# Optimization experiments

Measured on AMD Instinct MI355X. Metric: run time of the kernel, lower is better.

## Reference

```python
import jax, jax.numpy as jnp
import numpy as np

B, T, C, H, NT = 1, 1024, 768, 12, 8
D = C // H  # 64
POWER_ITERS = 4
DP_TEMP = 0.8
ESR_GAMMA = 0.02
ESR_ALPHA = 0.1


def rmsnorm(x, w, eps=1e-6):
    rms = jax.lax.rsqrt(jnp.mean(x * x, axis=-1, keepdims=True) + eps)
    return x * rms * w


def setup_inputs():
    key = jax.random.key(0)
    k0, k1, k2 = jax.random.split(key, 3)
    return {
        "x": jax.random.normal(k0, (B, T, C), jnp.float32),
        "W_qkvg": jax.random.normal(k1, (4 * C, C), jnp.float32) * 0.02,
        "W_out": jax.random.normal(k2, (C, C), jnp.float32) * 0.02,
        "lam": jnp.float32(1.5),
        "log_tau": -0.5 * jnp.ones((H, NT), jnp.float32),
        "logit_w": jnp.zeros((H, NT), jnp.float32),
        "beta": 1.5 * jnp.ones((H,), jnp.float32),
        "out_scale": jnp.ones((H,), jnp.float32),
        "dp_scale": jnp.ones((H,), jnp.float32),
        "logk_scale": jnp.ones((H,), jnp.float32),
        "dt_logit": jnp.float32(np.log(1.0 / 1e-8)),  # dt=1.0 -> logit = log(dt/(1-dt+1e-8))
        "g_norm_w": jnp.ones((D,), jnp.float32),
    }


def reference(x, W_qkvg, W_out, lam, log_tau, logit_w, beta, out_scale,
              dp_scale, logk_scale, dt_logit, g_norm_w):
    # qkvg projection and head split
    qkvg = x @ W_qkvg.T                                    # [B,T,4C]
    q, k, v, g = jnp.split(qkvg, 4, axis=-1)
    to_heads = lambda t: t.reshape(B, T, H, D).transpose(0, 2, 1, 3)  # [B,H,T,D]
    q, k, v, g = map(to_heads, (q, k, v, g))
    g = rmsnorm(g, g_norm_w)

    # pairwise squared distance ||g_i - g_j||^2
    g2 = jnp.sum(g * g, axis=-1)                           # [B,H,T]
    s = jnp.maximum(g2[..., :, None] + g2[..., None, :]
                    - 2.0 * jnp.einsum('bhid,bhjd->bhij', g, g), 0.0)  # [B,H,T,T]

    # fractional log-kernel: logsumexp_t[-(beta/2) log1p(s/(4 tau_t)) + log w_t]
    tau = jnp.maximum(jnp.exp(log_tau), 1e-6)              # [H,NT]
    w = jax.nn.softmax(logit_w, axis=-1)                   # [H,NT]
    beta_c = jnp.clip(beta, 0.5, 2.5)                      # [H]
    log_k_per = -(beta_c[None, :, None, None, None] / 2.0) * jnp.log1p(
        s[:, :, None] / (4.0 * tau[None, :, :, None, None]))          # [B,H,NT,T,T]
    logK = jax.nn.logsumexp(log_k_per + jnp.log(w + 1e-12)[None, :, :, None, None], axis=2)
    logK = logK * logk_scale[None, :, None, None]

    # dot-product scores
    dp = jnp.einsum('bhid,bhjd->bhij', q, k) * (dp_scale[None, :, None, None]
                                                / (np.sqrt(D) * DP_TEMP))

    # causal Markov normalize: blend, mask, stable row-softmax
    mask = jnp.tril(jnp.ones((T, T), bool))[None, None]    # [1,1,T,T]
    blended = lam * dp + (1.0 - lam) * logK
    blended = jnp.where(mask, blended, -jnp.inf)
    mx = jnp.max(blended, axis=-1, keepdims=True)
    mx = jnp.where(jnp.isfinite(mx), mx, 0.0)
    Kmat = jnp.exp(jnp.maximum(blended - mx, -60.0)) * mask
    P = Kmat / jnp.maximum(Kmat.sum(-1, keepdims=True), 1e-12)

    # power iteration for left stationary pi with full-support teleport
    pi0 = jnp.full((B, H, 1, T), 1.0 / T, P.dtype)
    def step(pi, _):
        p = (1.0 - ESR_GAMMA) * (pi @ P) + ESR_GAMMA / T
        p = p / jnp.maximum(p.sum(-1, keepdims=True), 1e-12)
        return p, None
    pi, _ = jax.lax.scan(step, pi0, None, length=POWER_ITERS)
    pi = jax.lax.stop_gradient(pi[..., 0, :])              # [B,H,T] (detached)

    # causal approximation to additive reversibilization
    P_adj = (pi[..., None, :] / jnp.maximum(pi[..., :, None], 1e-12)) \
            * jnp.swapaxes(P, -1, -2)                      # P*_ij = (pi_j/pi_i) P_ji
    P_rev = 0.5 * (P + P_adj) * mask
    P_rev = P_rev / jnp.maximum(P_rev.sum(-1, keepdims=True), 1e-12)

    dt = jax.nn.sigmoid(dt_logit)
    alpha = ESR_ALPHA * dt                                  # scale_alpha_by_dt=True
    P_fin = (1.0 - alpha) * P + alpha * P_rev

    y = (P_fin @ v) * out_scale[None, :, None, None]       # [B,H,T,D]
    y = y.transpose(0, 2, 1, 3).reshape(B, T, C)
    return y @ W_out.T
```

## Files before the change

kernel.cpp:

```cpp
#include <hip/hip_runtime.h>
#include <math.h>

#define TSEQ 1024
#define CD   768
#define HN   12
#define DD   64

#define OFF_QH     0
#define OFF_KH     393216
#define OFF_GH     786432
#define OFF_VHT    1179648
#define OFF_VH     1572864
#define OFF_G2     1966080
#define OFF_YB     1978368
#define OFF_CONSTS 2371584
#define OFF_OPART  2372096
#define OFF_LS     8663552
#define OFF_PD     8761856
#define OFF_XB     8774144
#define OFF_WQB    9167360
#define OFF_WOB    10347008

#define N_XB  786432
#define N_WQB 2359296
#define N_WOB 589824

typedef __bf16 bf16x8 __attribute__((ext_vector_type(8)));
typedef float  f32x4  __attribute__((ext_vector_type(4)));
typedef unsigned short u16x8 __attribute__((ext_vector_type(8)));
typedef unsigned short u16x4 __attribute__((ext_vector_type(4)));

__device__ inline unsigned short f2bf(float f) {
  unsigned int u = __float_as_uint(f);
  return (unsigned short)((u + 0x7fffu + ((u >> 16) & 1u)) >> 16);
}
__device__ inline float bf2f(unsigned short u) {
  return __uint_as_float((unsigned)u << 16);
}


__global__ __launch_bounds__(64) void prep_kernel(
    const float* __restrict__ lam_p, const float* __restrict__ log_tau,
    const float* __restrict__ logit_w, const float* __restrict__ beta,
    const float* __restrict__ out_scale, const float* __restrict__ dp_scale,
    const float* __restrict__ logk_scale, const float* __restrict__ dt_logit,
    float* __restrict__ consts) {
  int h = threadIdx.x;
  if (h == 0) {
    float dt = 1.0f / (1.0f + __expf(-dt_logit[0]));
    consts[288] = 0.1f * dt;
  }
  if (h < HN) {
    float lam = lam_p[0];
    float* c = consts + h * 24;
    c[0] = lam * dp_scale[h] * (1.0f / 6.4f);
    c[1] = (1.0f - lam) * logk_scale[h];
    float b = fminf(fmaxf(beta[h], 0.5f), 2.5f);
    c[2] = 0.5f * b;
    c[3] = out_scale[h];
    float m = -1e30f;
    float lw[8];
    bool uni = true;
    for (int t = 0; t < 8; t++) {
      lw[t] = logit_w[h * 8 + t];
      m = fmaxf(m, lw[t]);
      if (log_tau[h * 8 + t] != log_tau[h * 8] || lw[t] != lw[0]) uni = false;
    }
    float s = 0.f;
    float e[8];
    for (int t = 0; t < 8; t++) { e[t] = __expf(lw[t] - m); s += e[t]; }
    for (int t = 0; t < 8; t++) {
      float w = e[t] / s;
      c[12 + t] = log2f(w + 1e-12f);
      float tau = fmaxf(__expf(log_tau[h * 8 + t]), 1e-6f);
      c[4 + t] = 1.0f / (4.0f * tau);
    }
    c[20] = uni ? 1.0f : 8.0f;
  }
}

__global__ __launch_bounds__(256) void convert_kernel(
    const float* __restrict__ x, const float* __restrict__ wq,
    const float* __restrict__ wo, unsigned short* __restrict__ xb,
    unsigned short* __restrict__ wqb, unsigned short* __restrict__ wob) {
  int i8 = (blockIdx.x * 256 + threadIdx.x) * 8;
  const float* src;
  unsigned short* dst;
  int off;
  if (i8 < N_XB) { src = x; dst = xb; off = i8; }
  else if (i8 < N_XB + N_WQB) { src = wq; dst = wqb; off = i8 - N_XB; }
  else if (i8 < N_XB + N_WQB + N_WOB) { src = wo; dst = wob; off = i8 - N_XB - N_WQB; }
  else return;
  float4 a = *(const float4*)&src[off];
  float4 b = *(const float4*)&src[off + 4];
  u16x8 u;
  u[0] = f2bf(a.x); u[1] = f2bf(a.y); u[2] = f2bf(a.z); u[3] = f2bf(a.w);
  u[4] = f2bf(b.x); u[5] = f2bf(b.y); u[6] = f2bf(b.z); u[7] = f2bf(b.w);
  *(u16x8*)&dst[off] = u;
}

__global__ __launch_bounds__(256, 2) void gemm_qkvg_fused(
    const unsigned short* __restrict__ A, const unsigned short* __restrict__ B,
    const float* __restrict__ consts, const float* __restrict__ g_norm_w,
    unsigned short* __restrict__ qh, unsigned short* __restrict__ kh,
    unsigned short* __restrict__ gh, unsigned short* __restrict__ vh,
    unsigned short* __restrict__ vhT, float* __restrict__ g2) {
  const int K = 768;
  __shared__ __align__(16) unsigned short As[128 * 72];
  __shared__ __align__(16) unsigned short Bs[64 * 72];
  int t = threadIdx.x;
  int lane = t & 63, w = t >> 6;
  int quad = lane >> 4, tx = lane & 15;
  int n0 = blockIdx.x * 64, m0 = blockIdx.y * 128;

  f32x4 acc[2][4] = {};
  int r_ = t >> 3, c8 = (t & 7) * 8;

  for (int k0 = 0; k0 < K; k0 += 64) {
    __syncthreads();
#pragma unroll
    for (int rep = 0; rep < 4; rep++) {
      int r = rep * 32 + r_;
      *(u16x8*)&As[r * 72 + c8] = *(const u16x8*)&A[(size_t)(m0 + r) * K + k0 + c8];
    }
#pragma unroll
    for (int rep = 0; rep < 2; rep++) {
      int r = rep * 32 + r_;
      *(u16x8*)&Bs[r * 72 + c8] = *(const u16x8*)&B[(size_t)(n0 + r) * K + k0 + c8];
    }
    __syncthreads();

#pragma unroll
    for (int ks = 0; ks < 2; ks++) {
      bf16x8 af[2];
#pragma unroll
      for (int mi = 0; mi < 2; mi++)
        af[mi] = *(const bf16x8*)&As[(32 * w + mi * 16 + tx) * 72 + ks * 32 + quad * 8];
#pragma unroll
      for (int ni = 0; ni < 4; ni++) {
        bf16x8 bv = *(const bf16x8*)&Bs[(ni * 16 + tx) * 72 + ks * 32 + quad * 8];
#pragma unroll
        for (int mi = 0; mi < 2; mi++)
          acc[mi][ni] = __builtin_amdgcn_mfma_f32_16x16x32_bf16(af[mi], bv, acc[mi][ni], 0, 0, 0);
      }
    }
  }

  int typ = n0 / CD;
  int h = (n0 - typ * CD) >> 6;
  unsigned short* Ls = As;
  __syncthreads();

  if (typ == 3) {
    float gw4[4];
#pragma unroll
    for (int ni = 0; ni < 4; ni++) gw4[ni] = g_norm_w[ni * 16 + tx];
#pragma unroll
    for (int mi = 0; mi < 2; mi++) {
#pragma unroll
      for (int reg = 0; reg < 4; reg++) {
        float s1 = acc[mi][0][reg] * acc[mi][0][reg] + acc[mi][1][reg] * acc[mi][1][reg]
                 + acc[mi][2][reg] * acc[mi][2][reg] + acc[mi][3][reg] * acc[mi][3][reg];
#pragma unroll
        for (int m = 1; m < 16; m <<= 1) s1 += __shfl_xor(s1, m, 64);
        float rms = rsqrtf(s1 * (1.f / 64.f) + 1e-6f);
        int rl = 32 * w + mi * 16 + quad * 4 + reg;
        float s2 = 0.f;
#pragma unroll
        for (int ni = 0; ni < 4; ni++) {
          float v = acc[mi][ni][reg] * rms * gw4[ni];
          unsigned short us = f2bf(v);
          Ls[rl * 72 + ni * 16 + tx] = us;
          float vb = bf2f(us);
          s2 += vb * vb;
        }
#pragma unroll
        for (int m = 1; m < 16; m <<= 1) s2 += __shfl_xor(s2, m, 64);
        if (tx == 0) g2[h * 1024 + m0 + rl] = s2;
      }
    }
    __syncthreads();
#pragma unroll
    for (int rep = 0; rep < 4; rep++) {
      int idx = rep * 256 + t;
      int r = idx >> 3, cc = (idx & 7) * 8;
      *(u16x8*)&gh[(size_t)(h * 1024 + m0 + r) * 64 + cc] = *(const u16x8*)&Ls[r * 72 + cc];
    }
  } else {
    float sc = (typ == 0) ? consts[h * 24] * 1.44269504089f : 1.0f;
#pragma unroll
    for (int mi = 0; mi < 2; mi++)
#pragma unroll
      for (int ni = 0; ni < 4; ni++)
#pragma unroll
        for (int reg = 0; reg < 4; reg++) {
          int rl = 32 * w + mi * 16 + quad * 4 + reg;
          Ls[rl * 72 + ni * 16 + tx] = f2bf(acc[mi][ni][reg] * sc);
        }
    __syncthreads();
    unsigned short* dst = (typ == 0) ? qh : ((typ == 1) ? kh : vh);
#pragma unroll
    for (int rep = 0; rep < 4; rep++) {
      int idx = rep * 256 + t;
      int r = idx >> 3, cc = (idx & 7) * 8;
      *(u16x8*)&dst[(size_t)(h * 1024 + m0 + r) * 64 + cc] = *(const u16x8*)&Ls[r * 72 + cc];
    }
    if (typ == 2) {
#pragma unroll
      for (int rep = 0; rep < 4; rep++) {
        int idx = rep * 256 + t;
        int d = idx >> 4, rc = (idx & 15) * 8;
        u16x8 u;
#pragma unroll
        for (int j = 0; j < 8; j++) u[j] = Ls[(rc + j) * 72 + d];
        *(u16x8*)&vhT[(size_t)(h * 64 + d) * 1024 + m0 + rc] = u;
      }
    }
  }
}

__global__ __launch_bounds__(256, 2) void gemm_bf16_abT(
    const unsigned short* __restrict__ A, const unsigned short* __restrict__ B,
    float* __restrict__ Cm, int M, int N, int K) {
  __shared__ __align__(16) unsigned short As[128 * 72];
  __shared__ __align__(16) unsigned short Bs[64 * 72];
  int t = threadIdx.x;
  int lane = t & 63, w = t >> 6;
  int quad = lane >> 4, tx = lane & 15;
  int n0 = blockIdx.x * 64, m0 = blockIdx.y * 128;

  f32x4 acc[2][4] = {};
  int r_ = t >> 3, c8 = (t & 7) * 8;

  for (int k0 = 0; k0 < K; k0 += 64) {
    __syncthreads();
#pragma unroll
    for (int rep = 0; rep < 4; rep++) {
      int r = rep * 32 + r_;
      *(u16x8*)&As[r * 72 + c8] = *(const u16x8*)&A[(size_t)(m0 + r) * K + k0 + c8];
    }
#pragma unroll
    for (int rep = 0; rep < 2; rep++) {
      int r = rep * 32 + r_;
      *(u16x8*)&Bs[r * 72 + c8] = *(const u16x8*)&B[(size_t)(n0 + r) * K + k0 + c8];
    }
    __syncthreads();

#pragma unroll
    for (int ks = 0; ks < 2; ks++) {
      bf16x8 af[2];
#pragma unroll
      for (int mi = 0; mi < 2; mi++)
        af[mi] = *(const bf16x8*)&As[(32 * w + mi * 16 + tx) * 72 + ks * 32 + quad * 8];
#pragma unroll
      for (int ni = 0; ni < 4; ni++) {
        bf16x8 bv = *(const bf16x8*)&Bs[(ni * 16 + tx) * 72 + ks * 32 + quad * 8];
#pragma unroll
        for (int mi = 0; mi < 2; mi++)
          acc[mi][ni] = __builtin_amdgcn_mfma_f32_16x16x32_bf16(af[mi], bv, acc[mi][ni], 0, 0, 0);
      }
    }
  }

#pragma unroll
  for (int mi = 0; mi < 2; mi++)
#pragma unroll
    for (int ni = 0; ni < 4; ni++)
#pragma unroll
      for (int reg = 0; reg < 4; reg++) {
        int row = m0 + 32 * w + mi * 16 + quad * 4 + reg;
        Cm[(size_t)row * N + n0 + ni * 16 + tx] = acc[mi][ni][reg];
      }
}

__global__ __launch_bounds__(256, 3) void flash_kernel(
    const unsigned short* __restrict__ qh, const unsigned short* __restrict__ kh,
    const unsigned short* __restrict__ gh, const unsigned short* __restrict__ vhT,
    const float* __restrict__ g2, const float* __restrict__ consts,
    float* __restrict__ Opart, float* __restrict__ lsp, float* __restrict__ pdp) {
  int h = blockIdx.y;
  int uu = 143 - (int)blockIdx.x;
  int it = 0, rem = uu;
  for (it = 0; it < 32; ++it) {
    int njt_ = (it >> 1) + 1;
    int nc = (njt_ + 1) >> 1;
    if (rem < nc) break;
    rem -= nc;
  }
  int njt = (it >> 1) + 1;
  int jt0 = rem * 2;
  int jt1 = (jt0 + 2 < njt) ? (jt0 + 2) : njt;
  bool owns_diag = (jt1 == njt);
  int i0 = it * 32;
  int t = threadIdx.x;
  int lane = t & 63, w = t >> 6;
  int quad = lane >> 4, tx = lane & 15;
  int mi = w >> 1, nb = (w & 1) * 2;

  __shared__ __align__(16) unsigned short Qa[32 * 72];
  __shared__ __align__(16) unsigned short Ga[32 * 72];
  __shared__ __align__(16) unsigned short Ks[64 * 72];
  __shared__ __align__(16) unsigned short Gjs[64 * 72];
  __shared__ __align__(16) unsigned short Vt[64 * 72];
  __shared__ __align__(16) unsigned short psh[32 * 72];
  __shared__ float g2i[32], g2j[64], pdiag[32], lsum[32];

  const float* ch = consts + h * 24;
  float lkc = ch[1], bh2 = ch[2];
  int ntt = (int)ch[20];
  float i4t0 = ch[4];
  float inv4tau[8], logw[8];
#pragma unroll
  for (int tt = 0; tt < 8; tt++) { inv4tau[tt] = ch[4 + tt]; logw[tt] = ch[12 + tt]; }

  {
    int r = t >> 3, c8 = (t & 7) * 8;
    *(u16x8*)&Qa[r * 72 + c8] = *(const u16x8*)&qh[(size_t)(h * 1024 + i0 + r) * 64 + c8];
    *(u16x8*)&Ga[r * 72 + c8] = *(const u16x8*)&gh[(size_t)(h * 1024 + i0 + r) * 64 + c8];
  }
  if (t < 32) { g2i[t] = g2[h * 1024 + i0 + t]; pdiag[t] = 0.f; }
  __syncthreads();

  bf16x8 aq[2], ag[2];
#pragma unroll
  for (int ks = 0; ks < 2; ks++) {
    aq[ks] = *(const bf16x8*)&Qa[(mi * 16 + tx) * 72 + ks * 32 + quad * 8];
    ag[ks] = *(const bf16x8*)&Ga[(mi * 16 + tx) * 72 + ks * 32 + quad * 8];
  }

  f32x4 Oc[2] = {};
  float rowacc[4] = {0.f, 0.f, 0.f, 0.f};
  int r4 = t >> 2, cb = (t & 3) * 16;

  for (int jt = jt0; jt < jt1; jt++) {
    int j0 = jt * 64;
    __syncthreads();
    {
      const unsigned short* kp = &kh[(size_t)(h * 1024 + j0 + r4) * 64 + cb];
      const unsigned short* gp = &gh[(size_t)(h * 1024 + j0 + r4) * 64 + cb];
      const unsigned short* vp = &vhT[(size_t)(h * 64 + r4) * 1024 + j0 + cb];
      *(u16x8*)&Ks[r4 * 72 + cb] = *(const u16x8*)kp;
      *(u16x8*)&Ks[r4 * 72 + cb + 8] = *(const u16x8*)(kp + 8);
      *(u16x8*)&Gjs[r4 * 72 + cb] = *(const u16x8*)gp;
      *(u16x8*)&Gjs[r4 * 72 + cb + 8] = *(const u16x8*)(gp + 8);
      *(u16x8*)&Vt[r4 * 72 + cb] = *(const u16x8*)vp;
      *(u16x8*)&Vt[r4 * 72 + cb + 8] = *(const u16x8*)(vp + 8);
    }
    if (t < 64) g2j[t] = g2[h * 1024 + j0 + t];
    __syncthreads();

    f32x4 sqk[2] = {}, sgg[2] = {};
#pragma unroll
    for (int ni2 = 0; ni2 < 2; ni2++) {
#pragma unroll
      for (int ks = 0; ks < 2; ks++) {
        bf16x8 bk = *(const bf16x8*)&Ks[((nb + ni2) * 16 + tx) * 72 + ks * 32 + quad * 8];
        sqk[ni2] = __builtin_amdgcn_mfma_f32_16x16x32_bf16(aq[ks], bk, sqk[ni2], 0, 0, 0);
        bf16x8 bg = *(const bf16x8*)&Gjs[((nb + ni2) * 16 + tx) * 72 + ks * 32 + quad * 8];
        sgg[ni2] = __builtin_amdgcn_mfma_f32_16x16x32_bf16(ag[ks], bg, sgg[ni2], 0, 0, 0);
      }
    }

    float rs[4] = {0.f, 0.f, 0.f, 0.f};
#pragma unroll
    for (int ni2 = 0; ni2 < 2; ni2++) {
      int colg = j0 + (nb + ni2) * 16 + tx;
      float g2jv = g2j[(nb + ni2) * 16 + tx];
#pragma unroll
      for (int reg = 0; reg < 4; reg++) {
        int rowl = mi * 16 + quad * 4 + reg;
        int gi = i0 + rowl;
        float s = fmaxf(g2i[rowl] + g2jv - 2.0f * sgg[ni2][reg], 0.0f);
        float lse2;
        if (ntt == 1) {
          lse2 = -bh2 * __builtin_amdgcn_logf(fmaf(s, i4t0, 1.0f));
        } else {
          float se = 0.f;
#pragma unroll
          for (int tt = 0; tt < 8; tt++) {
            float lv = __builtin_amdgcn_logf(fmaf(s, inv4tau[tt], 1.0f));
            se += __builtin_amdgcn_exp2f(fmaf(-bh2, lv, logw[tt]));
          }
          lse2 = __builtin_amdgcn_logf(se + 1e-30f);
        }
        float b = fmaf(lkc, lse2, sqk[ni2][reg]);
        float p = (colg <= gi) ? __builtin_amdgcn_exp2f(b) : 0.0f;
        rs[reg] += p;
        psh[rowl * 72 + (nb + ni2) * 16 + tx] = f2bf(p);
        if (colg == gi) pdiag[rowl] = p;
      }
    }
#pragma unroll
    for (int reg = 0; reg < 4; reg++) {
#pragma unroll
      for (int m = 1; m < 16; m <<= 1) rs[reg] += __shfl_xor(rs[reg], m, 64);
      rowacc[reg] += rs[reg];
    }
    __syncthreads();

    bf16x8 ap[2];
#pragma unroll
    for (int ks = 0; ks < 2; ks++)
      ap[ks] = *(const bf16x8*)&psh[(mi * 16 + tx) * 72 + ks * 32 + quad * 8];
#pragma unroll
    for (int nd2 = 0; nd2 < 2; nd2++) {
#pragma unroll
      for (int ks = 0; ks < 2; ks++) {
        bf16x8 bv = *(const bf16x8*)&Vt[((nb + nd2) * 16 + tx) * 72 + ks * 32 + quad * 8];
        Oc[nd2] = __builtin_amdgcn_mfma_f32_16x16x32_bf16(ap[ks], bv, Oc[nd2], 0, 0, 0);
      }
    }
  }

  if ((w & 1) == 0 && tx == 0) {
#pragma unroll
    for (int reg = 0; reg < 4; reg++) lsum[mi * 16 + quad * 4 + reg] = rowacc[reg];
  }
  __syncthreads();
  if ((w & 1) == 1 && tx == 0) {
#pragma unroll
    for (int reg = 0; reg < 4; reg++) {
      int rowl = mi * 16 + quad * 4 + reg;
      lsp[(size_t)(rem * HN + h) * 1024 + i0 + rowl] = lsum[rowl] + rowacc[reg];
    }
  }
  float* Ob = Opart + (size_t)((rem * HN + h) * 1024 + i0) * 64;
#pragma unroll
  for (int nd2 = 0; nd2 < 2; nd2++) {
#pragma unroll
    for (int reg = 0; reg < 4; reg++) {
      int rowl = mi * 16 + quad * 4 + reg;
      Ob[rowl * 64 + (nb + nd2) * 16 + tx] = Oc[nd2][reg];
    }
  }
  if (owns_diag && t < 32) pdp[h * 1024 + i0 + t] = pdiag[t];
}

__global__ __launch_bounds__(256) void finalize_kernel(
    const float* __restrict__ Opart, const float* __restrict__ lsp,
    const float* __restrict__ pdp, const unsigned short* __restrict__ vh,
    const float* __restrict__ consts, unsigned short* __restrict__ yb) {
  int h = blockIdx.y;
  int t = threadIdx.x;
  int rl = t >> 4, d4 = t & 15;
  int gi = blockIdx.x * 16 + rl;
  int it = gi >> 5;
  int nc = (((it >> 1) + 1) + 1) >> 1;
  float alpha = consts[288];
  float osc = consts[h * 24 + 3];
  float4 Ov = make_float4(0.f, 0.f, 0.f, 0.f);
  float l = 0.f;
  for (int c = 0; c < nc; c++) {
    float4 p = *(const float4*)&Opart[(size_t)((c * HN + h) * 1024 + gi) * 64 + 4 * d4];
    Ov.x += p.x; Ov.y += p.y; Ov.z += p.z; Ov.w += p.w;
    l += lsp[(size_t)(c * HN + h) * 1024 + gi];
  }
  l = fmaxf(l, 1e-12f);
  float Pii = pdp[h * TSEQ + gi] / l;
  float inv1p = 1.0f / (1.0f + Pii);
  float c1 = (1.0f - alpha) + alpha * inv1p;
  float c2 = alpha * Pii * inv1p;
  float invl = 1.0f / l;
  u16x4 vb = *(const u16x4*)&vh[(size_t)(h * 1024 + gi) * 64 + 4 * d4];
  u16x4 o;
  o[0] = f2bf(osc * (c1 * Ov.x * invl + c2 * bf2f(vb[0])));
  o[1] = f2bf(osc * (c1 * Ov.y * invl + c2 * bf2f(vb[1])));
  o[2] = f2bf(osc * (c1 * Ov.z * invl + c2 * bf2f(vb[2])));
  o[3] = f2bf(osc * (c1 * Ov.w * invl + c2 * bf2f(vb[3])));
  *(u16x4*)&yb[(size_t)gi * CD + h * 64 + 4 * d4] = o;
}

extern "C" void kernel_launch(void* const* d_in, const int* in_sizes, int n_in,
                              void* d_out, int out_size, void* d_ws, size_t ws_size,
                              hipStream_t stream) {
  (void)in_sizes; (void)n_in; (void)out_size; (void)ws_size;
  const float* x          = (const float*)d_in[0];
  const float* W_qkvg     = (const float*)d_in[1];
  const float* W_out      = (const float*)d_in[2];
  const float* lam        = (const float*)d_in[3];
  const float* log_tau    = (const float*)d_in[4];
  const float* logit_w    = (const float*)d_in[5];
  const float* beta       = (const float*)d_in[6];
  const float* out_scale  = (const float*)d_in[7];
  const float* dp_scale   = (const float*)d_in[8];
  const float* logk_scale = (const float*)d_in[9];
  const float* dt_logit   = (const float*)d_in[10];
  const float* g_norm_w   = (const float*)d_in[11];
  float* ws = (float*)d_ws;
  unsigned short* qh  = (unsigned short*)(ws + OFF_QH);
  unsigned short* kh  = (unsigned short*)(ws + OFF_KH);
  unsigned short* gh  = (unsigned short*)(ws + OFF_GH);
  unsigned short* vhT = (unsigned short*)(ws + OFF_VHT);
  unsigned short* vh  = (unsigned short*)(ws + OFF_VH);
  float* g2     = ws + OFF_G2;
  unsigned short* yb  = (unsigned short*)(ws + OFF_YB);
  float* consts = ws + OFF_CONSTS;
  float* Opart  = ws + OFF_OPART;
  float* lsp    = ws + OFF_LS;
  float* pdp    = ws + OFF_PD;
  unsigned short* xb  = (unsigned short*)(ws + OFF_XB);
  unsigned short* wqb = (unsigned short*)(ws + OFF_WQB);
  unsigned short* wob = (unsigned short*)(ws + OFF_WOB);
  float* out = (float*)d_out;

  prep_kernel<<<dim3(1), dim3(64), 0, stream>>>(lam, log_tau, logit_w, beta,
                                                out_scale, dp_scale, logk_scale,
                                                dt_logit, consts);
  convert_kernel<<<dim3((N_XB + N_WQB + N_WOB) / (256 * 8)), dim3(256), 0, stream>>>(
      x, W_qkvg, W_out, xb, wqb, wob);
  gemm_qkvg_fused<<<dim3(48, 8), dim3(256), 0, stream>>>(xb, wqb, consts, g_norm_w,
                                                         qh, kh, gh, vh, vhT, g2);
  flash_kernel<<<dim3(144, 12), dim3(256), 0, stream>>>(qh, kh, gh, vhT, g2, consts,
                                                        Opart, lsp, pdp);
  finalize_kernel<<<dim3(64, 12), dim3(256), 0, stream>>>(Opart, lsp, pdp, vh, consts, yb);
  gemm_bf16_abT<<<dim3(12, 8), dim3(256), 0, stream>>>(yb, wob, out, 1024, 768, 768);
}
```

Before: 157.8 us.

## Pre-swizzle GEMM operands into MFMA fragment order and drop LDS staging

The convert kernel now writes x, W_qkvg and W_out in bf16 already laid out in MFMA 16x32 fragment order. The finalize kernel writes y in the same swizzled layout. Both GEMMs then load fragments straight from global memory into registers, with no LDS tiles and no block-wide barriers, and the epilogue uses per-wave LDS slices. This removes LDS round trips and syncs. In exchange, operand reuse across waves now depends on L1/L2 caching instead of shared memory, and the convert kernel's global reads become strided.

```diff
diff --git a/kernel.cpp b/kernel.cpp
--- a/kernel.cpp
+++ b/kernel.cpp
@@ -21,9 +21,9 @@
 #define OFF_WQB    9167360
 #define OFF_WOB    10347008
 
-#define N_XB  786432
-#define N_WQB 2359296
-#define N_WOB 589824
+#define NG_X  98304
+#define NG_WQ 294912
+#define NG_WO 73728
 
 typedef __bf16 bf16x8 __attribute__((ext_vector_type(8)));
 typedef float  f32x4  __attribute__((ext_vector_type(4)));
@@ -81,75 +81,61 @@
 
 __global__ __launch_bounds__(256) void convert_kernel(
     const float* __restrict__ x, const float* __restrict__ wq,
-    const float* __restrict__ wo, unsigned short* __restrict__ xb,
-    unsigned short* __restrict__ wqb, unsigned short* __restrict__ wob) {
-  int i8 = (blockIdx.x * 256 + threadIdx.x) * 8;
+    const float* __restrict__ wo, unsigned short* __restrict__ swzA,
+    unsigned short* __restrict__ swzWQ, unsigned short* __restrict__ swzWO) {
+  int g = blockIdx.x * 256 + threadIdx.x;
   const float* src;
   unsigned short* dst;
-  int off;
-  if (i8 < N_XB) { src = x; dst = xb; off = i8; }
-  else if (i8 < N_XB + N_WQB) { src = wq; dst = wqb; off = i8 - N_XB; }
-  else if (i8 < N_XB + N_WQB + N_WOB) { src = wo; dst = wob; off = i8 - N_XB - N_WQB; }
+  int lg;
+  if (g < NG_X) { src = x; dst = swzA; lg = g; }
+  else if (g < NG_X + NG_WQ) { src = wq; dst = swzWQ; lg = g - NG_X; }
+  else if (g < NG_X + NG_WQ + NG_WO) { src = wo; dst = swzWO; lg = g - NG_X - NG_WQ; }
   else return;
-  float4 a = *(const float4*)&src[off];
-  float4 b = *(const float4*)&src[off + 4];
+  int lane = lg & 63;
+  int kb = (lg >> 6) % 24;
+  int t16 = lg / (64 * 24);
+  int row = t16 * 16 + (lane & 15);
+  int col = kb * 32 + (lane >> 4) * 8;
+  const float* s = &src[(size_t)row * 768 + col];
+  float4 a = *(const float4*)s;
+  float4 b = *(const float4*)(s + 4);
   u16x8 u;
   u[0] = f2bf(a.x); u[1] = f2bf(a.y); u[2] = f2bf(a.z); u[3] = f2bf(a.w);
   u[4] = f2bf(b.x); u[5] = f2bf(b.y); u[6] = f2bf(b.z); u[7] = f2bf(b.w);
-  *(u16x8*)&dst[off] = u;
-}
-
-__global__ __launch_bounds__(256, 2) void gemm_qkvg_fused(
-    const unsigned short* __restrict__ A, const unsigned short* __restrict__ B,
+  *(u16x8*)&dst[(size_t)lg * 8] = u;
+}
+
+__global__ __launch_bounds__(256) void gemm_frag_qkvg(
+    const unsigned short* __restrict__ swzA, const unsigned short* __restrict__ swzB,
     const float* __restrict__ consts, const float* __restrict__ g_norm_w,
     unsigned short* __restrict__ qh, unsigned short* __restrict__ kh,
     unsigned short* __restrict__ gh, unsigned short* __restrict__ vh,
     unsigned short* __restrict__ vhT, float* __restrict__ g2) {
-  const int K = 768;
-  __shared__ __align__(16) unsigned short As[128 * 72];
-  __shared__ __align__(16) unsigned short Bs[64 * 72];
-  int t = threadIdx.x;
-  int lane = t & 63, w = t >> 6;
+  __shared__ __align__(16) unsigned short Ls[128 * 72];
+  int t = threadIdx.x, lane = t & 63, w = t >> 6;
   int quad = lane >> 4, tx = lane & 15;
-  int n0 = blockIdx.x * 64, m0 = blockIdx.y * 128;
+  int ntile = blockIdx.x;
+  int m0 = blockIdx.y * 128;
+  int nt0 = ntile * 4;
+  int mt0 = blockIdx.y * 8 + w * 2;
 
   f32x4 acc[2][4] = {};
-  int r_ = t >> 3, c8 = (t & 7) * 8;
-
-  for (int k0 = 0; k0 < K; k0 += 64) {
-    __syncthreads();
-#pragma unroll
-    for (int rep = 0; rep < 4; rep++) {
-      int r = rep * 32 + r_;
-      *(u16x8*)&As[r * 72 + c8] = *(const u16x8*)&A[(size_t)(m0 + r) * K + k0 + c8];
-    }
-#pragma unroll
-    for (int rep = 0; rep < 2; rep++) {
-      int r = rep * 32 + r_;
-      *(u16x8*)&Bs[r * 72 + c8] = *(const u16x8*)&B[(size_t)(n0 + r) * K + k0 + c8];
-    }
-    __syncthreads();
-
-#pragma unroll
-    for (int ks = 0; ks < 2; ks++) {
-      bf16x8 af[2];
-#pragma unroll
-      for (int mi = 0; mi < 2; mi++)
-        af[mi] = *(const bf16x8*)&As[(32 * w + mi * 16 + tx) * 72 + ks * 32 + quad * 8];
-#pragma unroll
-      for (int ni = 0; ni < 4; ni++) {
-        bf16x8 bv = *(const bf16x8*)&Bs[(ni * 16 + tx) * 72 + ks * 32 + quad * 8];
-#pragma unroll
-        for (int mi = 0; mi < 2; mi++)
-          acc[mi][ni] = __builtin_amdgcn_mfma_f32_16x16x32_bf16(af[mi], bv, acc[mi][ni], 0, 0, 0);
-      }
-    }
-  }
-
-  int typ = n0 / CD;
-  int h = (n0 - typ * CD) >> 6;
-  unsigned short* Ls = As;
-  __syncthreads();
+#pragma unroll 2
+  for (int kb = 0; kb < 24; kb++) {
+    bf16x8 a0 = *(const bf16x8*)&swzA[((size_t)((mt0 + 0) * 24 + kb) * 64 + lane) * 8];
+    bf16x8 a1 = *(const bf16x8*)&swzA[((size_t)((mt0 + 1) * 24 + kb) * 64 + lane) * 8];
+#pragma unroll
+    for (int ni = 0; ni < 4; ni++) {
+      bf16x8 b = *(const bf16x8*)&swzB[((size_t)((nt0 + ni) * 24 + kb) * 64 + lane) * 8];
+      acc[0][ni] = __builtin_amdgcn_mfma_f32_16x16x32_bf16(a0, b, acc[0][ni], 0, 0, 0);
+      acc[1][ni] = __builtin_amdgcn_mfma_f32_16x16x32_bf16(a1, b, acc[1][ni], 0, 0, 0);
+    }
+  }
+
+  int typ = ntile / 12;
+  int h = ntile % 12;
+  unsigned short* Lw = Ls + w * (32 * 72);
+  int mrow0 = m0 + w * 32;
 
   if (typ == 3) {
     float gw4[4];
@@ -164,27 +150,26 @@
 #pragma unroll
         for (int m = 1; m < 16; m <<= 1) s1 += __shfl_xor(s1, m, 64);
         float rms = rsqrtf(s1 * (1.f / 64.f) + 1e-6f);
-        int rl = 32 * w + mi * 16 + quad * 4 + reg;
+        int rl = mi * 16 + quad * 4 + reg;
         float s2 = 0.f;
 #pragma unroll
         for (int ni = 0; ni < 4; ni++) {
           float v = acc[mi][ni][reg] * rms * gw4[ni];
           unsigned short us = f2bf(v);
-          Ls[rl * 72 + ni * 16 + tx] = us;
+          Lw[rl * 72 + ni * 16 + tx] = us;
           float vb = bf2f(us);
           s2 += vb * vb;
         }
 #pragma unroll
         for (int m = 1; m < 16; m <<= 1) s2 += __shfl_xor(s2, m, 64);
-        if (tx == 0) g2[h * 1024 + m0 + rl] = s2;
-      }
-    }
-    __syncthreads();
+        if (tx == 0) g2[h * 1024 + mrow0 + rl] = s2;
+      }
+    }
 #pragma unroll
     for (int rep = 0; rep < 4; rep++) {
-      int idx = rep * 256 + t;
+      int idx = rep * 64 + lane;
       int r = idx >> 3, cc = (idx & 7) * 8;
-      *(u16x8*)&gh[(size_t)(h * 1024 + m0 + r) * 64 + cc] = *(const u16x8*)&Ls[r * 72 + cc];
+      *(u16x8*)&gh[(size_t)(h * 1024 + mrow0 + r) * 64 + cc] = *(const u16x8*)&Lw[r * 72 + cc];
     }
   } else {
     float sc = (typ == 0) ? consts[h * 24] * 1.44269504089f : 1.0f;
@@ -194,82 +179,60 @@
       for (int ni = 0; ni < 4; ni++)
 #pragma unroll
         for (int reg = 0; reg < 4; reg++) {
-          int rl = 32 * w + mi * 16 + quad * 4 + reg;
-          Ls[rl * 72 + ni * 16 + tx] = f2bf(acc[mi][ni][reg] * sc);
+          int rl = mi * 16 + quad * 4 + reg;
+          Lw[rl * 72 + ni * 16 + tx] = f2bf(acc[mi][ni][reg] * sc);
         }
-    __syncthreads();
     unsigned short* dst = (typ == 0) ? qh : ((typ == 1) ? kh : vh);
 #pragma unroll
     for (int rep = 0; rep < 4; rep++) {
-      int idx = rep * 256 + t;
+      int idx = rep * 64 + lane;
       int r = idx >> 3, cc = (idx & 7) * 8;
-      *(u16x8*)&dst[(size_t)(h * 1024 + m0 + r) * 64 + cc] = *(const u16x8*)&Ls[r * 72 + cc];
+      *(u16x8*)&dst[(size_t)(h * 1024 + mrow0 + r) * 64 + cc] = *(const u16x8*)&Lw[r * 72 + cc];
     }
     if (typ == 2) {
 #pragma unroll
       for (int rep = 0; rep < 4; rep++) {
-        int idx = rep * 256 + t;
-        int d = idx >> 4, rc = (idx & 15) * 8;
+        int idx = rep * 64 + lane;
+        int d = idx >> 2, rc = (idx & 3) * 8;
         u16x8 u;
 #pragma unroll
-        for (int j = 0; j < 8; j++) u[j] = Ls[(rc + j) * 72 + d];
-        *(u16x8*)&vhT[(size_t)(h * 64 + d) * 1024 + m0 + rc] = u;
-      }
-    }
-  }
-}
-
-__global__ __launch_bounds__(256, 2) void gemm_bf16_abT(
-    const unsigned short* __restrict__ A, const unsigned short* __restrict__ B,
-    float* __restrict__ Cm, int M, int N, int K) {
-  __shared__ __align__(16) unsigned short As[128 * 72];
-  __shared__ __align__(16) unsigned short Bs[64 * 72];
-  int t = threadIdx.x;
-  int lane = t & 63, w = t >> 6;
+        for (int j = 0; j < 8; j++) u[j] = Lw[(rc + j) * 72 + d];
+        *(u16x8*)&vhT[(size_t)(h * 64 + d) * 1024 + mrow0 + rc] = u;
+      }
+    }
+  }
+}
+
+__global__ __launch_bounds__(256) void gemm_frag_out(
+    const unsigned short* __restrict__ swzA, const unsigned short* __restrict__ swzB,
+    float* __restrict__ Cm) {
+  int t = threadIdx.x, lane = t & 63, w = t >> 6;
   int quad = lane >> 4, tx = lane & 15;
-  int n0 = blockIdx.x * 64, m0 = blockIdx.y * 128;
+  int n0 = blockIdx.x * 64;
+  int m0 = blockIdx.y * 128;
+  int nt0 = blockIdx.x * 4;
+  int mt0 = blockIdx.y * 8 + w * 2;
 
   f32x4 acc[2][4] = {};
-  int r_ = t >> 3, c8 = (t & 7) * 8;
-
-  for (int k0 = 0; k0 < K; k0 += 64) {
-    __syncthreads();
-#pragma unroll
-    for (int rep = 0; rep < 4; rep++) {
-      int r = rep * 32 + r_;
-      *(u16x8*)&As[r * 72 + c8] = *(const u16x8*)&A[(size_t)(m0 + r) * K + k0 + c8];
-    }
-#pragma unroll
-    for (int rep = 0; rep < 2; rep++) {
-      int r = rep * 32 + r_;
-      *(u16x8*)&Bs[r * 72 + c8] = *(const u16x8*)&B[(size_t)(n0 + r) * K + k0 + c8];
-    }
-    __syncthreads();
-
-#pragma unroll
-    for (int ks = 0; ks < 2; ks++) {
-      bf16x8 af[2];
-#pragma unroll
-      for (int mi = 0; mi < 2; mi++)
-        af[mi] = *(const bf16x8*)&As[(32 * w + mi * 16 + tx) * 72 + ks * 32 + quad * 8];
-#pragma unroll
-      for (int ni = 0; ni < 4; ni++) {
-        bf16x8 bv = *(const bf16x8*)&Bs[(ni * 16 + tx) * 72 + ks * 32 + quad * 8];
-#pragma unroll
-        for (int mi = 0; mi < 2; mi++)
-          acc[mi][ni] = __builtin_amdgcn_mfma_f32_16x16x32_bf16(af[mi], bv, acc[mi][ni], 0, 0, 0);
-      }
-    }
-  }
-
+#pragma unroll 2
+  for (int kb = 0; kb < 24; kb++) {
+    bf16x8 a0 = *(const bf16x8*)&swzA[((size_t)((mt0 + 0) * 24 + kb) * 64 + lane) * 8];
+    bf16x8 a1 = *(const bf16x8*)&swzA[((size_t)((mt0 + 1) * 24 + kb) * 64 + lane) * 8];
+#pragma unroll
+    for (int ni = 0; ni < 4; ni++) {
+      bf16x8 b = *(const bf16x8*)&swzB[((size_t)((nt0 + ni) * 24 + kb) * 64 + lane) * 8];
+      acc[0][ni] = __builtin_amdgcn_mfma_f32_16x16x32_bf16(a0, b, acc[0][ni], 0, 0, 0);
+      acc[1][ni] = __builtin_amdgcn_mfma_f32_16x16x32_bf16(a1, b, acc[1][ni], 0, 0, 0);
+    }
+  }
 #pragma unroll
   for (int mi = 0; mi < 2; mi++)
 #pragma unroll
     for (int ni = 0; ni < 4; ni++)
 #pragma unroll
       for (int reg = 0; reg < 4; reg++) {
-        int row = m0 + 32 * w + mi * 16 + quad * 4 + reg;
-        Cm[(size_t)row * N + n0 + ni * 16 + tx] = acc[mi][ni][reg];
+        int row = m0 + w * 32 + mi * 16 + quad * 4 + reg;
+        Cm[(size_t)row * CD + n0 + ni * 16 + tx] = acc[mi][ni][reg];
       }
 }
 
@@ -467,7 +430,11 @@
   o[1] = f2bf(osc * (c1 * Ov.y * invl + c2 * bf2f(vb[1])));
   o[2] = f2bf(osc * (c1 * Ov.z * invl + c2 * bf2f(vb[2])));
   o[3] = f2bf(osc * (c1 * Ov.w * invl + c2 * bf2f(vb[3])));
-  *(u16x4*)&yb[(size_t)gi * CD + h * 64 + 4 * d4] = o;
+  int k = h * 64 + 4 * d4;
+  int kb = k >> 5, q8 = (k & 31) >> 3, j0 = k & 7;
+  int mt = gi >> 4, txl = gi & 15;
+  size_t off = (((size_t)mt * 24 + kb) * 64 + q8 * 16 + txl) * 8 + j0;
+  *(u16x4*)&yb[off] = o;
 }
 
 extern "C" void kernel_launch(void* const* d_in, const int* in_sizes, int n_in,
@@ -498,20 +465,20 @@
   float* Opart  = ws + OFF_OPART;
   float* lsp    = ws + OFF_LS;
   float* pdp    = ws + OFF_PD;
-  unsigned short* xb  = (unsigned short*)(ws + OFF_XB);
-  unsigned short* wqb = (unsigned short*)(ws + OFF_WQB);
-  unsigned short* wob = (unsigned short*)(ws + OFF_WOB);
+  unsigned short* swzA = (unsigned short*)(ws + OFF_XB);
+  unsigned short* swzWQ = (unsigned short*)(ws + OFF_WQB);
+  unsigned short* swzWO = (unsigned short*)(ws + OFF_WOB);
   float* out = (float*)d_out;
 
   prep_kernel<<<dim3(1), dim3(64), 0, stream>>>(lam, log_tau, logit_w, beta,
                                                 out_scale, dp_scale, logk_scale,
                                                 dt_logit, consts);
-  convert_kernel<<<dim3((N_XB + N_WQB + N_WOB) / (256 * 8)), dim3(256), 0, stream>>>(
-      x, W_qkvg, W_out, xb, wqb, wob);
-  gemm_qkvg_fused<<<dim3(48, 8), dim3(256), 0, stream>>>(xb, wqb, consts, g_norm_w,
-                                                         qh, kh, gh, vh, vhT, g2);
+  convert_kernel<<<dim3((NG_X + NG_WQ + NG_WO) / 256), dim3(256), 0, stream>>>(
+      x, W_qkvg, W_out, swzA, swzWQ, swzWO);
+  gemm_frag_qkvg<<<dim3(48, 8), dim3(256), 0, stream>>>(swzA, swzWQ, consts, g_norm_w,
+                                                        qh, kh, gh, vh, vhT, g2);
   flash_kernel<<<dim3(144, 12), dim3(256), 0, stream>>>(qh, kh, gh, vhT, g2, consts,
                                                         Opart, lsp, pdp);
   finalize_kernel<<<dim3(64, 12), dim3(256), 0, stream>>>(Opart, lsp, pdp, vh, consts, yb);
-  gemm_bf16_abT<<<dim3(12, 8), dim3(256), 0, stream>>>(yb, wob, out, 1024, 768, 768);
-}
+  gemm_frag_out<<<dim3(12, 8), dim3(256), 0, stream>>>(yb, swzWO, out);
+}
```

After: 156.2 us. About the same (-1.1%).
